# Optimization experiments

Hardware: AMD Instinct MI355X
Metric: run time of the kernel (lower is better)

Reference implementation:

```python
import jax, jax.numpy as jnp
import numpy as np

N_HEADS = 4
N_GROUPS = 32
EPS = 1e-5


def setup_inputs() -> dict:
    key = jax.random.key(0)
    ks = jax.random.split(key, 6)
    c = 512
    x = jax.random.normal(ks[0], (4, c, 64, 64), dtype=jnp.float32)
    # conv1x1 weights ~ kaiming-ish scale
    s = 1.0 / np.sqrt(c)
    wq = jax.random.normal(ks[1], (c, c), dtype=jnp.float32) * s
    wk = jax.random.normal(ks[2], (c, c), dtype=jnp.float32) * s
    wv = jax.random.normal(ks[3], (c, c), dtype=jnp.float32) * s
    wp = jax.random.normal(ks[4], (c, c), dtype=jnp.float32) * s
    zeros = jnp.zeros((c,), dtype=jnp.float32)
    return {
        "x": x,
        "gn_w": jnp.ones((c,), dtype=jnp.float32), "gn_b": zeros,
        "wq": wq, "bq": zeros, "wk": wk, "bk": zeros,
        "wv": wv, "bv": zeros, "wp": wp, "bp": zeros,
    }


def _group_norm(x, w, b):
    bsz, c, h, wd = x.shape
    xg = x.reshape(bsz, N_GROUPS, c // N_GROUPS, h, wd)
    mean = xg.mean(axis=(2, 3, 4), keepdims=True)
    var = xg.var(axis=(2, 3, 4), keepdims=True)
    xg = (xg - mean) * jax.lax.rsqrt(var + EPS)
    x = xg.reshape(bsz, c, h, wd)
    return x * w[None, :, None, None] + b[None, :, None, None]


def _conv1x1(x, w, b):
    # x: (b,c,h,w), w: (out,in) -> (b,out,h,w)
    return jnp.einsum('bchw,oc->bohw', x, w) + b[None, :, None, None]


def reference(x, gn_w, gn_b, wq, bq, wk, bk, wv, bv, wp, bp):
    bsz, c, h, wd = x.shape
    hd = c // N_HEADS
    hw = h * wd
    x_n = _group_norm(x, gn_w, gn_b)
    q = _conv1x1(x_n, wq, bq)
    k = _conv1x1(x_n, wk, bk)
    v = _conv1x1(x_n, wv, bv)

    def to_heads(t):
        # (b,c,h,w) -> (b, n_heads, hw, head_dim)
        return t.reshape(bsz, N_HEADS, hd, hw).transpose(0, 1, 3, 2)

    q, k, v = to_heads(q), to_heads(k), to_heads(v)
    scale = hd ** (-0.5)
    attn = jnp.einsum('bhqd,bhkd->bhqk', q, k) * scale  # (b,H,hw,hw)
    attn = jax.nn.softmax(attn, axis=-1)
    out = jnp.einsum('bhqk,bhkd->bhqd', attn, v)
    out = out.transpose(0, 1, 3, 2).reshape(bsz, c, h, wd)
    out = _conv1x1(out, wp, bp)
    return x + out
```

## Files before the change

### kernel.cpp

```cpp
#include <hip/hip_runtime.h>
#include <math.h>

typedef __attribute__((ext_vector_type(8))) short short8;
typedef __attribute__((ext_vector_type(4))) float floatx4;
typedef __attribute__((ext_vector_type(16))) float floatx16;
typedef __attribute__((ext_vector_type(8))) unsigned short ushort8v;
typedef __attribute__((ext_vector_type(4))) unsigned short ushort4v;

#define HW 4096
#define CCH 512
#define NB 4
#define NH 4
#define HD 128

__device__ __forceinline__ unsigned short f2bf(float f) {
    union { float f; unsigned int u; } c; c.f = f;
    unsigned int u = c.u;
    u += 0x7FFFu + ((u >> 16) & 1u);
    return (unsigned short)(u >> 16);
}

__device__ __forceinline__ void gload_lds16(const unsigned short* g, unsigned short* l) {
    __builtin_amdgcn_global_load_lds(
        (const __attribute__((address_space(1))) unsigned int*)g,
        (__attribute__((address_space(3))) unsigned int*)l, 16, 0, 0);
}

__global__ void conv_w(const float* __restrict__ w0, const float* __restrict__ w1,
                       const float* __restrict__ w2, const float* __restrict__ w3,
                       unsigned short* __restrict__ dst) {
    const float* src = blockIdx.y == 0 ? w0 : blockIdx.y == 1 ? w1 : blockIdx.y == 2 ? w2 : w3;
    unsigned short* d = dst + (size_t)blockIdx.y * 262144;
    int i = blockIdx.x * 256 + threadIdx.x;
    float4 v = ((const float4*)src)[i];
    ushort4v o;
    o[0] = f2bf(v.x); o[1] = f2bf(v.y); o[2] = f2bf(v.z); o[3] = f2bf(v.w);
    ((ushort4v*)d)[i] = o;
}

__global__ void gn_stats(const float* __restrict__ x, float* __restrict__ stats) {
    int bg = blockIdx.x;
    int b = bg >> 5, g = bg & 31;
    const float4* p = (const float4*)(x + ((size_t)b * CCH + g * 16) * HW);
    float s = 0.f, ss = 0.f;
    for (int i = threadIdx.x; i < 16384; i += 256) {
        float4 v = p[i];
        s  += v.x + v.y + v.z + v.w;
        ss += v.x * v.x + v.y * v.y + v.z * v.z + v.w * v.w;
    }
    #pragma unroll
    for (int off = 32; off > 0; off >>= 1) {
        s  += __shfl_down(s, off, 64);
        ss += __shfl_down(ss, off, 64);
    }
    __shared__ float sm[4], sm2[4];
    int wid = threadIdx.x >> 6;
    if ((threadIdx.x & 63) == 0) { sm[wid] = s; sm2[wid] = ss; }
    __syncthreads();
    if (threadIdx.x == 0) {
        float ts = sm[0] + sm[1] + sm[2] + sm[3];
        float tss = sm2[0] + sm2[1] + sm2[2] + sm2[3];
        float mean = ts * (1.f / 65536.f);
        float var = tss * (1.f / 65536.f) - mean * mean;
        stats[bg * 2] = mean;
        stats[bg * 2 + 1] = rsqrtf(var + 1e-5f);
    }
}

__global__ void gn_apply(const float* __restrict__ x, const float* __restrict__ gnw,
                         const float* __restrict__ gnb, const float* __restrict__ stats,
                         unsigned short* __restrict__ xt) {
    int s = blockIdx.x * 256 + threadIdx.x;
    int g = blockIdx.y, b = blockIdx.z;
    float mean = stats[(b * 32 + g) * 2];
    float rstd = stats[(b * 32 + g) * 2 + 1];
    const float* xb = x + ((size_t)b * CCH + g * 16) * HW + s;
    unsigned short outv[16];
    #pragma unroll
    for (int cl = 0; cl < 16; cl++) {
        int c = g * 16 + cl;
        float v = xb[(size_t)cl * HW];
        v = (v - mean) * rstd * gnw[c] + gnb[c];
        outv[cl] = f2bf(v);
    }
    unsigned short* dst = xt + ((size_t)b * HW + s) * CCH + g * 16;
    *(ushort8v*)dst       = *(ushort8v*)&outv[0];
    *(ushort8v*)(dst + 8) = *(ushort8v*)&outv[8];
}

template <int MODE>
__global__ __launch_bounds__(256, 3) void gemm_nt(
    const unsigned short* __restrict__ A, long long aStride,
    const unsigned short* __restrict__ Bm, long long bStride,
    const float* __restrict__ bias, float scale,
    const float* __restrict__ resid, long long rStride,
    void* __restrict__ Cp, long long cStride, int ldc) {
    __shared__ __align__(16) unsigned short lA[128 * 64];
    __shared__ __align__(16) unsigned short lB[128 * 64];
    const int tid = threadIdx.x;
    const int lane = tid & 63;
    const int wid = tid >> 6;
    const int z = blockIdx.z;
    const unsigned short* Ab = A + (size_t)z * aStride + (size_t)blockIdx.x * 128 * 512;
    const unsigned short* Bb = Bm + (size_t)z * bStride + (size_t)blockIdx.y * 128 * 512;

    floatx4 acc[4][4];
    #pragma unroll
    for (int i = 0; i < 4; i++)
        #pragma unroll
        for (int j = 0; j < 4; j++) acc[i][j] = (floatx4)0.f;

    const int wm = (wid >> 1) * 64;
    const int wn = (wid & 1) * 64;
    const int l15 = lane & 15;
    const int l4 = lane >> 4;
    const int sxr = l15 & 7;

    size_t srcOff[4];
    int dstBase[4];
    #pragma unroll
    for (int n = 0; n < 4; n++) {
        int row = n * 32 + (tid >> 3);
        int g = tid & 7;
        srcOff[n] = (size_t)row * 512 + (size_t)((g ^ (row & 7)) << 3);
        dstBase[n] = (n * 256 + wid * 64) * 8;
    }

    #pragma unroll 1
    for (int t = 0; t < 8; t++) {
        int k0 = t * 64;
        #pragma unroll
        for (int n = 0; n < 4; n++) gload_lds16(&Ab[srcOff[n] + k0], lA + dstBase[n]);
        #pragma unroll
        for (int n = 0; n < 4; n++) gload_lds16(&Bb[srcOff[n] + k0], lB + dstBase[n]);
        __syncthreads();
        #pragma unroll
        for (int kk = 0; kk < 2; kk++) {
            short8 af[4], bf[4];
            #pragma unroll
            for (int i = 0; i < 4; i++)
                af[i] = *(const short8*)&lA[(wm + i * 16 + l15) * 64 + (((kk * 4 + l4) ^ sxr) << 3)];
            #pragma unroll
            for (int j = 0; j < 4; j++)
                bf[j] = *(const short8*)&lB[(wn + j * 16 + l15) * 64 + (((kk * 4 + l4) ^ sxr) << 3)];
            #pragma unroll
            for (int i = 0; i < 4; i++)
                #pragma unroll
                for (int j = 0; j < 4; j++)
                    acc[i][j] = __builtin_amdgcn_mfma_f32_16x16x32_bf16(af[i], bf[j], acc[i][j], 0, 0, 0);
        }
        if (t < 7) __syncthreads();
    }

    long long m0 = (long long)blockIdx.x * 128 + wm;
    long long n0 = (long long)blockIdx.y * 128 + wn;
    if (MODE == 0 || MODE == 3) {
        unsigned short* C = (unsigned short*)Cp + (size_t)z * cStride;
        const float* bptr = (MODE == 3 && z == 1) ? resid : bias;
        float sc = (MODE == 3 && z == 1) ? 1.f : scale;
        #pragma unroll
        for (int i = 0; i < 4; i++)
            #pragma unroll
            for (int j = 0; j < 4; j++) {
                long long col = n0 + j * 16 + l15;
                float bv = bptr[col];
                #pragma unroll
                for (int r = 0; r < 4; r++) {
                    long long row = m0 + i * 16 + l4 * 4 + r;
                    C[row * ldc + col] = f2bf((acc[i][j][r] + bv) * sc);
                }
            }
    } else if (MODE == 1) {
        float* C = (float*)Cp + (size_t)z * cStride;
        const float* R = resid + (size_t)z * rStride;
        #pragma unroll
        for (int i = 0; i < 4; i++)
            #pragma unroll
            for (int j = 0; j < 4; j++)
                #pragma unroll
                for (int r = 0; r < 4; r++) {
                    long long row = m0 + i * 16 + l4 * 4 + r;
                    long long col = n0 + j * 16 + l15;
                    C[row * ldc + col] = acc[i][j][r] + bias[row] + R[row * ldc + col];
                }
    } else {
        unsigned short* C = (unsigned short*)Cp + (size_t)z * cStride;
        #pragma unroll
        for (int i = 0; i < 4; i++)
            #pragma unroll
            for (int j = 0; j < 4; j++)
                #pragma unroll
                for (int r = 0; r < 4; r++) {
                    long long row = m0 + i * 16 + l4 * 4 + r;
                    long long col = n0 + j * 16 + l15;
                    C[row * ldc + col] = f2bf(acc[i][j][r] + bias[row]);
                }
    }
}

__global__ __launch_bounds__(512, 2) void attn_kern(
    const unsigned short* __restrict__ Qb, const unsigned short* __restrict__ Kb,
    const unsigned short* __restrict__ Vt, unsigned short* __restrict__ Ob) {
    __shared__ __align__(16) unsigned short lk0[8192], lk1[8192];
    __shared__ __align__(16) unsigned short lv0[8192], lv1[8192];
    const int tid = threadIdx.x;
    const int lane = tid & 63;
    const int w = tid >> 6;
    const int l31 = lane & 31;
    const int l1 = lane >> 5;
    const int bid = blockIdx.x;
    const int g = bid & 15;
    const int qt = bid >> 4;
    const int h = g & 3, b = g >> 2;
    const int q0 = qt * 256;
    const size_t headOff = (size_t)h * HD;
    const size_t batchRow = (size_t)b * HW;
    const unsigned short* VtB = Vt + ((size_t)b * CCH + headOff) * HW;

    size_t kSrc[2], vSrc[2];
    #pragma unroll
    for (int n = 0; n < 2; n++) {
        int row = w * 8 + n * 4 + (lane >> 4);
        int sk = ((row & 7) << 1) | ((row >> 3) & 1);
        int jk = (lane & 15) ^ sk;
        kSrc[n] = (batchRow + row) * 512 + headOff + jk * 8;
        int d = w * 16 + n * 8 + (lane >> 3);
        int jv = (lane & 7) ^ (d & 7);
        vSrc[n] = (size_t)d * HW + jv * 8;
    }
    const int ldsOff = w * 1024;

    const int sk0 = ((l31 & 7) << 1) | ((l31 >> 3) & 1);
    const int sv0 = l31 & 7;

    short8 qf[8];
    #pragma unroll
    for (int kd = 0; kd < 8; kd++)
        qf[kd] = *(const short8*)&Qb[(batchRow + q0 + w * 32 + l31) * 512
                                     + headOff + kd * 16 + l1 * 8];

    short8 onesf;
    #pragma unroll
    for (int e = 0; e < 8; e++) onesf[e] = (short)0x3F80;

    floatx16 acc_o[4];
    floatx16 acc_l;
    acc_l = (floatx16)0.f;
    #pragma unroll
    for (int dj = 0; dj < 4; dj++) acc_o[dj] = (floatx16)0.f;

    #pragma unroll
    for (int n = 0; n < 2; n++) gload_lds16(&Kb[kSrc[n]], lk0 + ldsOff + n * 512);
    #pragma unroll
    for (int n = 0; n < 2; n++) gload_lds16(&Kb[kSrc[n] + (size_t)64 * 512], lk1 + ldsOff + n * 512);
    #pragma unroll
    for (int n = 0; n < 2; n++) gload_lds16(&VtB[vSrc[n]], lv0 + ldsOff + n * 512);
    __syncthreads();

    floatx16 sa0 = (floatx16)0.f, sa1 = (floatx16)0.f;
    #pragma unroll
    for (int kd = 0; kd < 8; kd++) {
        int xk = ((kd * 2 + l1) ^ sk0) * 8;
        short8 kf0 = *(const short8*)&lk0[l31 * 128 + xk];
        short8 kf1 = *(const short8*)&lk0[l31 * 128 + xk + 4096];
        sa0 = __builtin_amdgcn_mfma_f32_32x32x16_bf16(kf0, qf[kd], sa0, 0, 0, 0);
        sa1 = __builtin_amdgcn_mfma_f32_32x32x16_bf16(kf1, qf[kd], sa1, 0, 0, 0);
    }
    __syncthreads();

    unsigned short* lvCur = lv0;  unsigned short* lvNxt = lv1;
    unsigned short* kRead = lk1;  unsigned short* kWrite = lk0;

    #pragma unroll 1
    for (int kt = 0; kt < 63; kt++) {
        {
            size_t tv = (size_t)(kt + 1) * 64;
            size_t tk = (size_t)(kt + 2) * 64 * 512;
            #pragma unroll
            for (int n = 0; n < 2; n++) gload_lds16(&VtB[vSrc[n] + tv], lvNxt + ldsOff + n * 512);
            #pragma unroll
            for (int n = 0; n < 2; n++) gload_lds16(&Kb[kSrc[n] + tk], kWrite + ldsOff + n * 512);
        }

        short8 paf[4];
        #pragma unroll
        for (int r = 0; r < 16; r++) sa0[r] = __builtin_amdgcn_exp2f(sa0[r]);
        #pragma unroll
        for (int r = 0; r < 16; r++) sa1[r] = __builtin_amdgcn_exp2f(sa1[r]);
        #pragma unroll
        for (int tb = 0; tb < 2; tb++) {
            const floatx16& sa = tb ? sa1 : sa0;
            unsigned int wv[4][2];
            #pragma unroll
            for (int gg = 0; gg < 4; gg++) {
                asm("v_cvt_pk_bf16_f32 %0, %1, %2" : "=v"(wv[gg][0])
                    : "v"(sa[4 * gg + 0]), "v"(sa[4 * gg + 1]));
                asm("v_cvt_pk_bf16_f32 %0, %1, %2" : "=v"(wv[gg][1])
                    : "v"(sa[4 * gg + 2]), "v"(sa[4 * gg + 3]));
            }
            #pragma unroll
            for (int hh = 0; hh < 2; hh++) {
                unsigned int a0 = wv[2 * hh][0], b0 = wv[2 * hh + 1][0];
                unsigned int a1 = wv[2 * hh][1], b1 = wv[2 * hh + 1][1];
                asm("v_permlane32_swap_b32 %0, %1" : "+v"(a0), "+v"(b0));
                asm("v_permlane32_swap_b32 %0, %1" : "+v"(a1), "+v"(b1));
                union { unsigned int u[4]; short8 s8; } f;
                f.u[0] = a0; f.u[1] = a1; f.u[2] = b0; f.u[3] = b1;
                paf[2 * tb + hh] = f.s8;
            }
        }

        sa0 = (floatx16)0.f; sa1 = (floatx16)0.f;
        __builtin_amdgcn_s_setprio(1);
        #pragma unroll
        for (int u = 0; u < 4; u++) {
            #pragma unroll
            for (int q2 = 0; q2 < 2; q2++) {
                int kd = u * 2 + q2;
                int xk = ((kd * 2 + l1) ^ sk0) * 8;
                short8 kf0 = *(const short8*)&kRead[l31 * 128 + xk];
                short8 kf1 = *(const short8*)&kRead[l31 * 128 + xk + 4096];
                sa0 = __builtin_amdgcn_mfma_f32_32x32x16_bf16(kf0, qf[kd], sa0, 0, 0, 0);
                sa1 = __builtin_amdgcn_mfma_f32_32x32x16_bf16(kf1, qf[kd], sa1, 0, 0, 0);
            }
            acc_l = __builtin_amdgcn_mfma_f32_32x32x16_bf16(paf[u], onesf, acc_l, 0, 0, 0);
            int xv = ((u * 2 + l1) ^ sv0) * 8;
            #pragma unroll
            for (int dj = 0; dj < 4; dj++) {
                short8 vv = *(const short8*)&lvCur[dj * 2048 + l31 * 64 + xv];
                acc_o[dj] = __builtin_amdgcn_mfma_f32_32x32x16_bf16(paf[u], vv, acc_o[dj], 0, 0, 0);
            }
        }
        __builtin_amdgcn_s_setprio(0);

        __syncthreads();
        unsigned short* t;
        t = lvCur; lvCur = lvNxt; lvNxt = t;
        t = kRead; kRead = kWrite; kWrite = t;
    }

    {
        short8 paf[4];
        #pragma unroll
        for (int r = 0; r < 16; r++) sa0[r] = __builtin_amdgcn_exp2f(sa0[r]);
        #pragma unroll
        for (int r = 0; r < 16; r++) sa1[r] = __builtin_amdgcn_exp2f(sa1[r]);
        #pragma unroll
        for (int tb = 0; tb < 2; tb++) {
            const floatx16& sa = tb ? sa1 : sa0;
            unsigned int wv[4][2];
            #pragma unroll
            for (int gg = 0; gg < 4; gg++) {
                asm("v_cvt_pk_bf16_f32 %0, %1, %2" : "=v"(wv[gg][0])
                    : "v"(sa[4 * gg + 0]), "v"(sa[4 * gg + 1]));
                asm("v_cvt_pk_bf16_f32 %0, %1, %2" : "=v"(wv[gg][1])
                    : "v"(sa[4 * gg + 2]), "v"(sa[4 * gg + 3]));
            }
            #pragma unroll
            for (int hh = 0; hh < 2; hh++) {
                unsigned int a0 = wv[2 * hh][0], b0 = wv[2 * hh + 1][0];
                unsigned int a1 = wv[2 * hh][1], b1 = wv[2 * hh + 1][1];
                asm("v_permlane32_swap_b32 %0, %1" : "+v"(a0), "+v"(b0));
                asm("v_permlane32_swap_b32 %0, %1" : "+v"(a1), "+v"(b1));
                union { unsigned int u[4]; short8 s8; } f;
                f.u[0] = a0; f.u[1] = a1; f.u[2] = b0; f.u[3] = b1;
                paf[2 * tb + hh] = f.s8;
            }
        }
        __builtin_amdgcn_s_setprio(1);
        #pragma unroll
        for (int u = 0; u < 4; u++) {
            acc_l = __builtin_amdgcn_mfma_f32_32x32x16_bf16(paf[u], onesf, acc_l, 0, 0, 0);
            int xv = ((u * 2 + l1) ^ sv0) * 8;
            #pragma unroll
            for (int dj = 0; dj < 4; dj++) {
                short8 vv = *(const short8*)&lvCur[dj * 2048 + l31 * 64 + xv];
                acc_o[dj] = __builtin_amdgcn_mfma_f32_32x32x16_bf16(paf[u], vv, acc_o[dj], 0, 0, 0);
            }
        }
        __builtin_amdgcn_s_setprio(0);
    }

    #pragma unroll
    for (int gg = 0; gg < 4; gg++)
        #pragma unroll
        for (int p = 0; p < 4; p++) {
            int reg = 4 * gg + p;
            float rl = 1.f / acc_l[reg];
            int qr = p + 8 * gg + 4 * l1;
            size_t row = batchRow + q0 + w * 32 + qr;
            #pragma unroll
            for (int dj = 0; dj < 4; dj++)
                Ob[row * 512 + headOff + dj * 32 + l31] = f2bf(acc_o[dj][reg] * rl);
        }
}

extern "C" void kernel_launch(void* const* d_in, const int* in_sizes, int n_in,
                              void* d_out, int out_size, void* d_ws, size_t ws_size,
                              hipStream_t stream) {
    const float* x   = (const float*)d_in[0];
    const float* gnw = (const float*)d_in[1];
    const float* gnb = (const float*)d_in[2];
    const float* wq  = (const float*)d_in[3];
    const float* bq  = (const float*)d_in[4];
    const float* wk  = (const float*)d_in[5];
    const float* bk  = (const float*)d_in[6];
    const float* wv  = (const float*)d_in[7];
    const float* bv  = (const float*)d_in[8];
    const float* wp  = (const float*)d_in[9];
    const float* bp  = (const float*)d_in[10];
    float* out = (float*)d_out;

    const size_t NE = (size_t)NB * HW * CCH;
    unsigned short* ws16 = (unsigned short*)d_ws;
    unsigned short* XT = ws16;
    unsigned short* Qb = ws16 + NE;
    unsigned short* Kb = ws16 + 2 * NE;
    unsigned short* Vt = ws16 + 3 * NE;
    unsigned short* Wb = ws16 + 4 * NE;
    float* stats = (float*)(ws16 + 4 * NE + 4 * 262144);

    const float qscale = 0.08838834764831845f * 1.4426950408889634f;

    conv_w<<<dim3(256, 4), 256, 0, stream>>>(wq, wk, wv, wp, Wb);
    gn_stats<<<128, 256, 0, stream>>>(x, stats);
    gn_apply<<<dim3(16, 32, 4), 256, 0, stream>>>(x, gnw, gnb, stats, XT);

    gemm_nt<3><<<dim3(128, 4, 2), 256, 0, stream>>>(XT, 0, Wb, 262144, bq, qscale, bk, 0,
                                                    Qb, (long long)NE, 512);
    gemm_nt<2><<<dim3(4, 32, 4), 256, 0, stream>>>(Wb + 2 * 262144, 0, XT, (long long)HW * 512, bv, 1.f,
                                                   nullptr, 0, Vt, (long long)CCH * HW, HW);

    unsigned short* Ob = XT;
    attn_kern<<<dim3(256), dim3(512), 0, stream>>>(Qb, Kb, Vt, Ob);

    gemm_nt<1><<<dim3(4, 32, 4), 256, 0, stream>>>(Wb + 3 * 262144, 0, Ob, (long long)HW * 512, bp, 1.f,
                                                   x, (long long)CCH * HW, out, (long long)CCH * HW, HW);
}
```

Before: 327.5 us.

## Write K and V in MFMA-fragment-packed tile layout for contiguous attention loads

The K and V projection epilogues now scatter their outputs into a per-(batch,head) tiled layout, so each 64-key tile the attention kernel streams becomes a contiguous 16 KB block laid out in MFMA fragment order. The attention kernel then issues linear global-to-LDS loads and reads fragments with simple strided LDS addressing instead of XOR-swizzled row/column gathers. This is meant to make the global loads fully coalesced and drop the swizzle arithmetic. In exchange the GEMM epilogue stores become scattered 2-byte writes, and LDS reads may see bank conflicts without the swizzle.

```diff
diff --git a/kernel.cpp b/kernel.cpp
--- a/kernel.cpp
+++ b/kernel.cpp
@@ -154,20 +154,38 @@
 
     long long m0 = (long long)blockIdx.x * 128 + wm;
     long long n0 = (long long)blockIdx.y * 128 + wn;
-    if (MODE == 0 || MODE == 3) {
-        unsigned short* C = (unsigned short*)Cp + (size_t)z * cStride;
-        const float* bptr = (MODE == 3 && z == 1) ? resid : bias;
-        float sc = (MODE == 3 && z == 1) ? 1.f : scale;
+    if (MODE == 3 && blockIdx.z == 1) {
+        unsigned short* C = (unsigned short*)Cp + (size_t)cStride;
         #pragma unroll
         for (int i = 0; i < 4; i++)
             #pragma unroll
             for (int j = 0; j < 4; j++) {
                 long long col = n0 + j * 16 + l15;
-                float bv = bptr[col];
+                float bv = resid[col];
+                int hh = (int)(col >> 7);
+                int d = (int)(col & 127);
+                size_t dpart = (size_t)(d >> 3) * 512 + (size_t)(d & 7);
                 #pragma unroll
                 for (int r = 0; r < 4; r++) {
                     long long row = m0 + i * 16 + l4 * 4 + r;
-                    C[row * ldc + col] = f2bf((acc[i][j][r] + bv) * sc);
+                    int bb = (int)(row >> 12), s = (int)(row & 4095);
+                    size_t addr = (size_t)(bb * NH + hh) * 524288
+                                + (size_t)(s >> 6) * 8192 + dpart + (size_t)(s & 63) * 8;
+                    C[addr] = f2bf(acc[i][j][r] + bv);
+                }
+            }
+    } else if (MODE == 0 || MODE == 3) {
+        unsigned short* C = (unsigned short*)Cp + (size_t)z * cStride;
+        #pragma unroll
+        for (int i = 0; i < 4; i++)
+            #pragma unroll
+            for (int j = 0; j < 4; j++) {
+                long long col = n0 + j * 16 + l15;
+                float bv = bias[col];
+                #pragma unroll
+                for (int r = 0; r < 4; r++) {
+                    long long row = m0 + i * 16 + l4 * 4 + r;
+                    C[row * ldc + col] = f2bf((acc[i][j][r] + bv) * scale);
                 }
             }
     } else if (MODE == 1) {
@@ -184,7 +202,8 @@
                     C[row * ldc + col] = acc[i][j][r] + bias[row] + R[row * ldc + col];
                 }
     } else {
-        unsigned short* C = (unsigned short*)Cp + (size_t)z * cStride;
+        unsigned short* C = (unsigned short*)Cp;
+        const int b = z;
         #pragma unroll
         for (int i = 0; i < 4; i++)
             #pragma unroll
@@ -193,14 +212,20 @@
                 for (int r = 0; r < 4; r++) {
                     long long row = m0 + i * 16 + l4 * 4 + r;
                     long long col = n0 + j * 16 + l15;
-                    C[row * ldc + col] = f2bf(acc[i][j][r] + bias[row]);
+                    int hh = (int)(row >> 7);
+                    int d = (int)(row & 127);
+                    int s = (int)col;
+                    size_t addr = (size_t)(b * NH + hh) * 524288
+                                + (size_t)(s >> 6) * 8192
+                                + (size_t)(((s & 63) >> 3) * 128 + d) * 8 + (size_t)(s & 7);
+                    C[addr] = f2bf(acc[i][j][r] + bias[row]);
                 }
     }
 }
 
 __global__ __launch_bounds__(512, 2) void attn_kern(
-    const unsigned short* __restrict__ Qb, const unsigned short* __restrict__ Kb,
-    const unsigned short* __restrict__ Vt, unsigned short* __restrict__ Ob) {
+    const unsigned short* __restrict__ Qb, const unsigned short* __restrict__ Kp,
+    const unsigned short* __restrict__ Vp, unsigned short* __restrict__ Ob) {
     __shared__ __align__(16) unsigned short lk0[8192], lk1[8192];
     __shared__ __align__(16) unsigned short lv0[8192], lv1[8192];
     const int tid = threadIdx.x;
@@ -215,23 +240,11 @@
     const int q0 = qt * 256;
     const size_t headOff = (size_t)h * HD;
     const size_t batchRow = (size_t)b * HW;
-    const unsigned short* VtB = Vt + ((size_t)b * CCH + headOff) * HW;
-
-    size_t kSrc[2], vSrc[2];
-    #pragma unroll
-    for (int n = 0; n < 2; n++) {
-        int row = w * 8 + n * 4 + (lane >> 4);
-        int sk = ((row & 7) << 1) | ((row >> 3) & 1);
-        int jk = (lane & 15) ^ sk;
-        kSrc[n] = (batchRow + row) * 512 + headOff + jk * 8;
-        int d = w * 16 + n * 8 + (lane >> 3);
-        int jv = (lane & 7) ^ (d & 7);
-        vSrc[n] = (size_t)d * HW + jv * 8;
-    }
+    const unsigned short* KpB = Kp + (size_t)(b * NH + h) * 524288;
+    const unsigned short* VpB = Vp + (size_t)(b * NH + h) * 524288;
+
+    const size_t dmaOff = (size_t)(w * 128 + lane) * 8;
     const int ldsOff = w * 1024;
-
-    const int sk0 = ((l31 & 7) << 1) | ((l31 >> 3) & 1);
-    const int sv0 = l31 & 7;
 
     short8 qf[8];
     #pragma unroll
@@ -250,19 +263,18 @@
     for (int dj = 0; dj < 4; dj++) acc_o[dj] = (floatx16)0.f;
 
     #pragma unroll
-    for (int n = 0; n < 2; n++) gload_lds16(&Kb[kSrc[n]], lk0 + ldsOff + n * 512);
-    #pragma unroll
-    for (int n = 0; n < 2; n++) gload_lds16(&Kb[kSrc[n] + (size_t)64 * 512], lk1 + ldsOff + n * 512);
-    #pragma unroll
-    for (int n = 0; n < 2; n++) gload_lds16(&VtB[vSrc[n]], lv0 + ldsOff + n * 512);
+    for (int n = 0; n < 2; n++) gload_lds16(&KpB[dmaOff + n * 512], lk0 + ldsOff + n * 512);
+    #pragma unroll
+    for (int n = 0; n < 2; n++) gload_lds16(&KpB[dmaOff + 8192 + n * 512], lk1 + ldsOff + n * 512);
+    #pragma unroll
+    for (int n = 0; n < 2; n++) gload_lds16(&VpB[dmaOff + n * 512], lv0 + ldsOff + n * 512);
     __syncthreads();
 
     floatx16 sa0 = (floatx16)0.f, sa1 = (floatx16)0.f;
     #pragma unroll
     for (int kd = 0; kd < 8; kd++) {
-        int xk = ((kd * 2 + l1) ^ sk0) * 8;
-        short8 kf0 = *(const short8*)&lk0[l31 * 128 + xk];
-        short8 kf1 = *(const short8*)&lk0[l31 * 128 + xk + 4096];
+        short8 kf0 = *(const short8*)&lk0[(kd * 2 + l1) * 512 + l31 * 8];
+        short8 kf1 = *(const short8*)&lk0[(kd * 2 + l1) * 512 + 256 + l31 * 8];
         sa0 = __builtin_amdgcn_mfma_f32_32x32x16_bf16(kf0, qf[kd], sa0, 0, 0, 0);
         sa1 = __builtin_amdgcn_mfma_f32_32x32x16_bf16(kf1, qf[kd], sa1, 0, 0, 0);
     }
@@ -274,12 +286,12 @@
     #pragma unroll 1
     for (int kt = 0; kt < 63; kt++) {
         {
-            size_t tv = (size_t)(kt + 1) * 64;
-            size_t tk = (size_t)(kt + 2) * 64 * 512;
-            #pragma unroll
-            for (int n = 0; n < 2; n++) gload_lds16(&VtB[vSrc[n] + tv], lvNxt + ldsOff + n * 512);
-            #pragma unroll
-            for (int n = 0; n < 2; n++) gload_lds16(&Kb[kSrc[n] + tk], kWrite + ldsOff + n * 512);
+            size_t tv = (size_t)(kt + 1) * 8192;
+            size_t tk = (size_t)(kt + 2) * 8192;
+            #pragma unroll
+            for (int n = 0; n < 2; n++) gload_lds16(&VpB[dmaOff + tv + n * 512], lvNxt + ldsOff + n * 512);
+            #pragma unroll
+            for (int n = 0; n < 2; n++) gload_lds16(&KpB[dmaOff + tk + n * 512], kWrite + ldsOff + n * 512);
         }
 
         short8 paf[4];
@@ -317,17 +329,15 @@
             #pragma unroll
             for (int q2 = 0; q2 < 2; q2++) {
                 int kd = u * 2 + q2;
-                int xk = ((kd * 2 + l1) ^ sk0) * 8;
-                short8 kf0 = *(const short8*)&kRead[l31 * 128 + xk];
-                short8 kf1 = *(const short8*)&kRead[l31 * 128 + xk + 4096];
+                short8 kf0 = *(const short8*)&kRead[(kd * 2 + l1) * 512 + l31 * 8];
+                short8 kf1 = *(const short8*)&kRead[(kd * 2 + l1) * 512 + 256 + l31 * 8];
                 sa0 = __builtin_amdgcn_mfma_f32_32x32x16_bf16(kf0, qf[kd], sa0, 0, 0, 0);
                 sa1 = __builtin_amdgcn_mfma_f32_32x32x16_bf16(kf1, qf[kd], sa1, 0, 0, 0);
             }
             acc_l = __builtin_amdgcn_mfma_f32_32x32x16_bf16(paf[u], onesf, acc_l, 0, 0, 0);
-            int xv = ((u * 2 + l1) ^ sv0) * 8;
             #pragma unroll
             for (int dj = 0; dj < 4; dj++) {
-                short8 vv = *(const short8*)&lvCur[dj * 2048 + l31 * 64 + xv];
+                short8 vv = *(const short8*)&lvCur[(u * 2 + l1) * 1024 + dj * 256 + l31 * 8];
                 acc_o[dj] = __builtin_amdgcn_mfma_f32_32x32x16_bf16(paf[u], vv, acc_o[dj], 0, 0, 0);
             }
         }
@@ -371,10 +381,9 @@
         #pragma unroll
         for (int u = 0; u < 4; u++) {
             acc_l = __builtin_amdgcn_mfma_f32_32x32x16_bf16(paf[u], onesf, acc_l, 0, 0, 0);
-            int xv = ((u * 2 + l1) ^ sv0) * 8;
             #pragma unroll
             for (int dj = 0; dj < 4; dj++) {
-                short8 vv = *(const short8*)&lvCur[dj * 2048 + l31 * 64 + xv];
+                short8 vv = *(const short8*)&lvCur[(u * 2 + l1) * 1024 + dj * 256 + l31 * 8];
                 acc_o[dj] = __builtin_amdgcn_mfma_f32_32x32x16_bf16(paf[u], vv, acc_o[dj], 0, 0, 0);
             }
         }
@@ -429,7 +438,7 @@
     gemm_nt<3><<<dim3(128, 4, 2), 256, 0, stream>>>(XT, 0, Wb, 262144, bq, qscale, bk, 0,
                                                     Qb, (long long)NE, 512);
     gemm_nt<2><<<dim3(4, 32, 4), 256, 0, stream>>>(Wb + 2 * 262144, 0, XT, (long long)HW * 512, bv, 1.f,
-                                                   nullptr, 0, Vt, (long long)CCH * HW, HW);
+                                                   nullptr, 0, Vt, 0, HW);
 
     unsigned short* Ob = XT;
     attn_kern<<<dim3(256), dim3(512), 0, stream>>>(Qb, Kb, Vt, Ob);
```

Result: no change. 322.0 us (-1.7%).
